# Performance work log

Measured on AMD Instinct MI355X. Metric: run time of the kernel, lower is better.

Reference implementation:

```python
import jax, jax.numpy as jnp
import numpy as np

B, S, D = 4, 2048, 16
N_HEAD_ARG = 16
# Faithful to source bug: effective num heads = hidden_size (D), head_size = D // n_head_arg.
# This only type-checks when head_size == 1 (D == n_head_arg), as in the repo config.
HEADS = D                     # self.n_head = hidden_size
HEAD_SIZE = D // N_HEAD_ARG   # = 1


def setup_inputs() -> dict:
    key = jax.random.key(0)
    k_x, k_wq, k_bq, k_wo, k_bo = jax.random.split(key, 5)
    x = jax.random.normal(k_x, (B, S, D), dtype=jnp.float32)
    # torch Linear init scale ~ 1/sqrt(in_features); store weights as [in, out]
    s = 1.0 / np.sqrt(D)
    w_qkv = jax.random.uniform(k_wq, (D, 3 * D), minval=-s, maxval=s, dtype=jnp.float32)
    b_qkv = jax.random.uniform(k_bq, (3 * D,), minval=-s, maxval=s, dtype=jnp.float32)
    w_out = jax.random.uniform(k_wo, (D, D), minval=-s, maxval=s, dtype=jnp.float32)
    b_out = jax.random.uniform(k_bo, (D,), minval=-s, maxval=s, dtype=jnp.float32)
    return {"x": x, "w_qkv": w_qkv, "b_qkv": b_qkv, "w_out": w_out, "b_out": b_out}


def reference(x, w_qkv, b_qkv, w_out, b_out):
    b, s, _ = x.shape
    qkv = x @ w_qkv + b_qkv                      # [b, s, 3D]
    q, k, v = jnp.split(qkv, 3, axis=-1)         # each [b, s, D]
    # [b, s, H, hs] -> [b, H, s, hs]
    q = q.reshape(b, s, HEADS, HEAD_SIZE).transpose(0, 2, 1, 3)
    k = k.reshape(b, s, HEADS, HEAD_SIZE).transpose(0, 2, 1, 3)
    v = v.reshape(b, s, HEADS, HEAD_SIZE).transpose(0, 2, 1, 3)
    scale = 1.0 / jnp.sqrt(jnp.asarray(HEAD_SIZE, dtype=x.dtype))
    scores = jnp.einsum('bhqd,bhkd->bhqk', q, k) * scale   # [b, H, s, s]
    causal = jnp.tril(jnp.ones((s, s), dtype=bool))
    scores = jnp.where(causal, scores, jnp.asarray(-jnp.inf, dtype=scores.dtype))
    attn = jax.nn.softmax(scores, axis=-1)
    # dropout is identity in eval mode (correctness baseline)
    out = jnp.einsum('bhqk,bhkd->bhqd', attn, v)            # [b, H, s, hs]
    out = out.transpose(0, 2, 1, 3).reshape(b, s, HEADS * HEAD_SIZE)
    return out @ w_out + b_out
```

## Files before the change

kernel.cpp:

```cpp
#include <hip/hip_runtime.h>
#include <math.h>

#define BB 4
#define SS 2048
#define DD 16
#define HH 16
#define NM 32

#define EXP2(x) __builtin_amdgcn_exp2f(x)
#define LOG2E 1.44269504088896340736f

__constant__ float INVFACT[NM] = {
    1.000000000e+00f, 1.000000000e+00f, 5.000000000e-01f, 1.666666667e-01f,
    4.166666667e-02f, 8.333333333e-03f, 1.388888889e-03f, 1.984126984e-04f,
    2.480158730e-05f, 2.755731922e-06f, 2.755731922e-07f, 2.505210839e-08f,
    2.087675699e-09f, 1.605904384e-10f, 1.147074560e-11f, 7.647163732e-13f,
    4.779477332e-14f, 2.811457254e-15f, 1.561920697e-16f, 8.220635247e-18f,
    4.110317623e-19f, 1.957294106e-20f, 8.896791392e-22f, 3.868170171e-23f,
    1.611737571e-24f, 6.446950284e-26f, 2.479596263e-27f, 9.183689864e-29f,
    3.279889237e-30f, 1.130996289e-31f, 3.769987629e-33f, 1.216125042e-34f};

#define UNPACK16(X4, XR)                                                   \
  const float4 x0_ = (X4)[0], x1_ = (X4)[1], x2_ = (X4)[2], x3_ = (X4)[3]; \
  const float XR[16] = {x0_.x, x0_.y, x0_.z, x0_.w, x1_.x, x1_.y, x1_.z,   \
                        x1_.w, x2_.x, x2_.y, x2_.z, x2_.w, x3_.x, x3_.y,   \
                        x3_.z, x3_.w};

__global__ __launch_bounds__(256) void moment_kernel(
    const float* __restrict__ x, const float* __restrict__ w_qkv,
    const float* __restrict__ b_qkv, float* __restrict__ MT) {
  __shared__ float kl[512];
  __shared__ float vl[512];
  const int blk = blockIdx.x;
  const int sub = blk & 3;
  const int bh = blk >> 2;
  const int b = bh >> 4, h = bh & 15;
  const int t = threadIdx.x;

  float wk[16], wv[16];
#pragma unroll
  for (int i = 0; i < 16; ++i) {
    wk[i] = w_qkv[i * 48 + 16 + h];
    wv[i] = w_qkv[i * 48 + 32 + h];
  }
  const float bk = b_qkv[16 + h], bv = b_qkv[32 + h];

#pragma unroll
  for (int rr = 0; rr < 2; ++rr) {
    const int jl = rr * 256 + t;
    const int j = sub * 512 + jl;
    const float4* X4 = (const float4*)(x + ((size_t)b * SS + j) * DD);
    UNPACK16(X4, xr);
    float k = bk, v = bv;
#pragma unroll
    for (int i = 0; i < 16; ++i) {
      k = fmaf(xr[i], wk[i], k);
      v = fmaf(xr[i], wv[i], v);
    }
    kl[jl] = k;
    vl[jl] = v;
  }
  __syncthreads();

  const int m = t & 31;
  const int jl = t >> 5;
  const int jb = sub * 8 + jl;
  float s = 0.f, tv = 0.f;
  const int base = jl * 64;
  for (int u = 0; u < 64; ++u) {
    const float k = kl[base + u];
    const float v = vl[base + u];
    const float k2 = k * k, k4 = k2 * k2, k8 = k4 * k4, k16 = k8 * k8;
    float p = (m & 1) ? k : 1.f;
    p *= (m & 2) ? k2 : 1.f;
    p *= (m & 4) ? k4 : 1.f;
    p *= (m & 8) ? k8 : 1.f;
    p *= (m & 16) ? k16 : 1.f;
    s += p;
    tv = fmaf(p, v, tv);
  }
  float* row = MT + ((size_t)bh * 32 + jb) * 64;
  row[m] = s;
  row[32 + m] = tv;
}

__global__ __launch_bounds__(64) void attn_kernel(
    const float* __restrict__ x, const float* __restrict__ w_qkv,
    const float* __restrict__ b_qkv, const float* __restrict__ MT,
    float* __restrict__ AO) {
  __shared__ float kd[64], vd[64], bc[64];
  const int blk = blockIdx.x;
  const int qb = blk & 31;
  const int bh = blk >> 5;
  const int b = bh >> 4, h = bh & 15;
  const int lane = threadIdx.x;

  float wq[16], wk[16], wv[16];
#pragma unroll
  for (int i = 0; i < 16; ++i) {
    wq[i] = w_qkv[i * 48 + h];
    wk[i] = w_qkv[i * 48 + 16 + h];
    wv[i] = w_qkv[i * 48 + 32 + h];
  }

  const int i0 = qb * 64 + lane;
  const float4* X4 = (const float4*)(x + ((size_t)b * SS + i0) * DD);
  UNPACK16(X4, xr);
  float q = b_qkv[h], k = b_qkv[16 + h], v = b_qkv[32 + h];
#pragma unroll
  for (int i = 0; i < 16; ++i) {
    q = fmaf(xr[i], wq[i], q);
    k = fmaf(xr[i], wk[i], k);
    v = fmaf(xr[i], wv[i], v);
  }
  kd[lane] = k;
  vd[lane] = v;
  const float qs = q * LOG2E;

  if (qb > 0) {
    const float* mtb = MT + (size_t)bh * 32 * 64 + lane;
    float acc = 0.f;
    for (int jb = 0; jb < qb; ++jb) acc += mtb[jb * 64];
    const float c = INVFACT[lane & 31];
    const int slot = (lane < 32) ? (2 * lane) : (2 * (lane - 32) + 1);
    bc[slot] = acc * c;
  }
  __syncthreads();

  float num = 0.f, den = 0.f;
  if (qb > 0) {
    const float2* bc2 = (const float2*)bc;
    float p = 1.f;
#pragma unroll
    for (int m = 0; m < NM; ++m) {
      const float2 st = bc2[m];
      den = fmaf(p, st.x, den);
      num = fmaf(p, st.y, num);
      p *= q;
    }
  }

  float ld = 0.f, ad = 0.f;
  const float4* kd4 = (const float4*)kd;
  const float4* vd4 = (const float4*)vd;
#pragma unroll
  for (int g = 0; g < 16; ++g) {
    const float4 k4 = kd4[g], v4 = vd4[g];
    const int jj = 4 * g;
    float e;
    e = EXP2(qs * k4.x); e = (jj + 0 <= lane) ? e : 0.f; ld += e; ad = fmaf(e, v4.x, ad);
    e = EXP2(qs * k4.y); e = (jj + 1 <= lane) ? e : 0.f; ld += e; ad = fmaf(e, v4.y, ad);
    e = EXP2(qs * k4.z); e = (jj + 2 <= lane) ? e : 0.f; ld += e; ad = fmaf(e, v4.z, ad);
    e = EXP2(qs * k4.w); e = (jj + 3 <= lane) ? e : 0.f; ld += e; ad = fmaf(e, v4.w, ad);
  }

  AO[(size_t)bh * SS + i0] = (ad + num) / (ld + den);
}

__global__ __launch_bounds__(256) void proj_kernel(
    const float* __restrict__ AO, const float* __restrict__ w,
    const float* __restrict__ bias, float* __restrict__ out) {
  __shared__ float wct[DD * 68];
  __shared__ float aol[256];
  __shared__ float bs[DD];
  const int t = threadIdx.x;
  const int b = blockIdx.x >> 7;
  const int s_base = (blockIdx.x * 16) & (SS - 1);

  wct[(t & 15) * 68 + (t >> 4)] = w[t];
  if (t < DD) bs[t] = bias[t];
  {
    const int h = t >> 4, row_l = t & 15;
    const int bh = b * HH + h;
    aol[row_l * 16 + h] = AO[(size_t)bh * SS + s_base + row_l];
  }
  __syncthreads();

  const int row_l = t >> 4, d = t & 15;
  const float4* ao4 = (const float4*)aol;
  const float4* wc4 = (const float4*)wct;

  float y = bs[d];
#pragma unroll
  for (int g = 0; g < 4; ++g) {
    const float4 xv = ao4[row_l * 4 + g];
    const float4 wv = wc4[d * 17 + g];
    y = fmaf(xv.x, wv.x, y);
    y = fmaf(xv.y, wv.y, y);
    y = fmaf(xv.z, wv.z, y);
    y = fmaf(xv.w, wv.w, y);
  }
  out[(size_t)blockIdx.x * 256 + t] = y;
}

extern "C" void kernel_launch(void* const* d_in, const int* in_sizes, int n_in,
                              void* d_out, int out_size, void* d_ws,
                              size_t ws_size, hipStream_t stream) {
  const float* x = (const float*)d_in[0];
  const float* w_qkv = (const float*)d_in[1];
  const float* b_qkv = (const float*)d_in[2];
  const float* w_out = (const float*)d_in[3];
  const float* b_out = (const float*)d_in[4];
  float* out = (float*)d_out;

  float* ws = (float*)d_ws;
  float* MT = ws;
  float* AO = ws + 64 * 32 * 64;

  moment_kernel<<<256, 256, 0, stream>>>(x, w_qkv, b_qkv, MT);
  attn_kernel<<<2048, 64, 0, stream>>>(x, w_qkv, b_qkv, MT, AO);
  proj_kernel<<<512, 256, 0, stream>>>(AO, w_out, b_out, out);
}
```

Baseline: 80.37 us.

## Fuse moment and attention kernels into one block per batch-head with LDS prefix scan

Merges the moment-computation kernel and the attention kernel into a single kernel where each 1024-thread block handles one (batch, head) pair. Q/K/V projections are computed once into shared memory, per-chunk Taylor moments are built there, and a Hillis-Steele prefix scan over chunks replaces the per-query-block global re-summation. This removes one launch, the MT round trip through global memory and the redundant recomputation of K/V per query block. The cost is only 64 blocks on a GPU with many more compute units, so most of the device sits idle.

```diff
diff --git a/kernel.cpp b/kernel.cpp
--- a/kernel.cpp
+++ b/kernel.cpp
@@ -26,135 +26,117 @@
                         x1_.w, x2_.x, x2_.y, x2_.z, x2_.w, x3_.x, x3_.y,   \
                         x3_.z, x3_.w};
 
-__global__ __launch_bounds__(256) void moment_kernel(
+__global__ __launch_bounds__(1024) void fused_attn_kernel(
     const float* __restrict__ x, const float* __restrict__ w_qkv,
-    const float* __restrict__ b_qkv, float* __restrict__ MT) {
-  __shared__ float kl[512];
-  __shared__ float vl[512];
-  const int blk = blockIdx.x;
-  const int sub = blk & 3;
-  const int bh = blk >> 2;
+    const float* __restrict__ b_qkv, float* __restrict__ AO) {
+  __shared__ float kl[SS];
+  __shared__ float vl[SS];
+  __shared__ float ql[SS];
+  __shared__ float2 SP[32 * 32];
+
+  const int bh = blockIdx.x;
   const int b = bh >> 4, h = bh & 15;
   const int t = threadIdx.x;
 
-  float wk[16], wv[16];
-#pragma unroll
-  for (int i = 0; i < 16; ++i) {
-    wk[i] = w_qkv[i * 48 + 16 + h];
-    wv[i] = w_qkv[i * 48 + 32 + h];
-  }
-  const float bk = b_qkv[16 + h], bv = b_qkv[32 + h];
-
-#pragma unroll
-  for (int rr = 0; rr < 2; ++rr) {
-    const int jl = rr * 256 + t;
-    const int j = sub * 512 + jl;
-    const float4* X4 = (const float4*)(x + ((size_t)b * SS + j) * DD);
-    UNPACK16(X4, xr);
-    float k = bk, v = bv;
+  {
+    float wq[16], wk[16], wv[16];
 #pragma unroll
     for (int i = 0; i < 16; ++i) {
-      k = fmaf(xr[i], wk[i], k);
-      v = fmaf(xr[i], wv[i], v);
+      wq[i] = w_qkv[i * 48 + h];
+      wk[i] = w_qkv[i * 48 + 16 + h];
+      wv[i] = w_qkv[i * 48 + 32 + h];
     }
-    kl[jl] = k;
-    vl[jl] = v;
+    const float bq = b_qkv[h], bk = b_qkv[16 + h], bv = b_qkv[32 + h];
+#pragma unroll
+    for (int rr = 0; rr < 2; ++rr) {
+      const int j = rr * 1024 + t;
+      const float4* X4 = (const float4*)(x + ((size_t)b * SS + j) * DD);
+      UNPACK16(X4, xr);
+      float qq = bq, kk = bk, vv = bv;
+#pragma unroll
+      for (int i = 0; i < 16; ++i) {
+        qq = fmaf(xr[i], wq[i], qq);
+        kk = fmaf(xr[i], wk[i], kk);
+        vv = fmaf(xr[i], wv[i], vv);
+      }
+      ql[j] = qq;
+      kl[j] = kk;
+      vl[j] = vv;
+    }
   }
   __syncthreads();
 
-  const int m = t & 31;
-  const int jl = t >> 5;
-  const int jb = sub * 8 + jl;
-  float s = 0.f, tv = 0.f;
-  const int base = jl * 64;
-  for (int u = 0; u < 64; ++u) {
-    const float k = kl[base + u];
-    const float v = vl[base + u];
-    const float k2 = k * k, k4 = k2 * k2, k8 = k4 * k4, k16 = k8 * k8;
-    float p = (m & 1) ? k : 1.f;
-    p *= (m & 2) ? k2 : 1.f;
-    p *= (m & 4) ? k4 : 1.f;
-    p *= (m & 8) ? k8 : 1.f;
-    p *= (m & 16) ? k16 : 1.f;
-    s += p;
-    tv = fmaf(p, v, tv);
-  }
-  float* row = MT + ((size_t)bh * 32 + jb) * 64;
-  row[m] = s;
-  row[32 + m] = tv;
-}
-
-__global__ __launch_bounds__(64) void attn_kernel(
-    const float* __restrict__ x, const float* __restrict__ w_qkv,
-    const float* __restrict__ b_qkv, const float* __restrict__ MT,
-    float* __restrict__ AO) {
-  __shared__ float kd[64], vd[64], bc[64];
-  const int blk = blockIdx.x;
-  const int qb = blk & 31;
-  const int bh = blk >> 5;
-  const int b = bh >> 4, h = bh & 15;
-  const int lane = threadIdx.x;
-
-  float wq[16], wk[16], wv[16];
-#pragma unroll
-  for (int i = 0; i < 16; ++i) {
-    wq[i] = w_qkv[i * 48 + h];
-    wk[i] = w_qkv[i * 48 + 16 + h];
-    wv[i] = w_qkv[i * 48 + 32 + h];
-  }
-
-  const int i0 = qb * 64 + lane;
-  const float4* X4 = (const float4*)(x + ((size_t)b * SS + i0) * DD);
-  UNPACK16(X4, xr);
-  float q = b_qkv[h], k = b_qkv[16 + h], v = b_qkv[32 + h];
-#pragma unroll
-  for (int i = 0; i < 16; ++i) {
-    q = fmaf(xr[i], wq[i], q);
-    k = fmaf(xr[i], wk[i], k);
-    v = fmaf(xr[i], wv[i], v);
-  }
-  kd[lane] = k;
-  vd[lane] = v;
-  const float qs = q * LOG2E;
-
-  if (qb > 0) {
-    const float* mtb = MT + (size_t)bh * 32 * 64 + lane;
-    float acc = 0.f;
-    for (int jb = 0; jb < qb; ++jb) acc += mtb[jb * 64];
-    const float c = INVFACT[lane & 31];
-    const int slot = (lane < 32) ? (2 * lane) : (2 * (lane - 32) + 1);
-    bc[slot] = acc * c;
+  {
+    const int m = t & 31;
+    const int jb = t >> 5;
+    const float c = INVFACT[m];
+    float s = 0.f, tv = 0.f;
+    const int base = jb * 64;
+    for (int u = 0; u < 64; ++u) {
+      const float k = kl[base + u];
+      const float v = vl[base + u];
+      const float k2 = k * k, k4 = k2 * k2, k8 = k4 * k4, k16 = k8 * k8;
+      float p = (m & 1) ? k : 1.f;
+      p *= (m & 2) ? k2 : 1.f;
+      p *= (m & 4) ? k4 : 1.f;
+      p *= (m & 8) ? k8 : 1.f;
+      p *= (m & 16) ? k16 : 1.f;
+      s += p;
+      tv = fmaf(p, v, tv);
+    }
+    SP[t] = make_float2(s * c, tv * c);
   }
   __syncthreads();
 
-  float num = 0.f, den = 0.f;
-  if (qb > 0) {
-    const float2* bc2 = (const float2*)bc;
-    float p = 1.f;
+  {
+    const int jb = t >> 5;
 #pragma unroll
-    for (int m = 0; m < NM; ++m) {
-      const float2 st = bc2[m];
-      den = fmaf(p, st.x, den);
-      num = fmaf(p, st.y, num);
-      p *= q;
+    for (int off = 1; off < 32; off <<= 1) {
+      const float2 self = SP[t];
+      float2 othr = make_float2(0.f, 0.f);
+      if (jb >= off) othr = SP[t - off * 32];
+      __syncthreads();
+      SP[t] = make_float2(self.x + othr.x, self.y + othr.y);
+      __syncthreads();
     }
   }
 
-  float ld = 0.f, ad = 0.f;
-  const float4* kd4 = (const float4*)kd;
-  const float4* vd4 = (const float4*)vd;
+  for (int rr = 0; rr < 2; ++rr) {
+    const int i = rr * 1024 + t;
+    const int lane = i & 63;
+    const int qb = i >> 6;
+    const float q = ql[i];
+    const float qs = q * LOG2E;
+
+    float num = 0.f, den = 0.f;
+    if (qb > 0) {
+      const float2* bc2 = SP + (size_t)(qb - 1) * 32;
+      float p = 1.f;
 #pragma unroll
-  for (int g = 0; g < 16; ++g) {
-    const float4 k4 = kd4[g], v4 = vd4[g];
-    const int jj = 4 * g;
-    float e;
-    e = EXP2(qs * k4.x); e = (jj + 0 <= lane) ? e : 0.f; ld += e; ad = fmaf(e, v4.x, ad);
-    e = EXP2(qs * k4.y); e = (jj + 1 <= lane) ? e : 0.f; ld += e; ad = fmaf(e, v4.y, ad);
-    e = EXP2(qs * k4.z); e = (jj + 2 <= lane) ? e : 0.f; ld += e; ad = fmaf(e, v4.z, ad);
-    e = EXP2(qs * k4.w); e = (jj + 3 <= lane) ? e : 0.f; ld += e; ad = fmaf(e, v4.w, ad);
+      for (int m = 0; m < NM; ++m) {
+        const float2 st = bc2[m];
+        den = fmaf(p, st.x, den);
+        num = fmaf(p, st.y, num);
+        p *= q;
+      }
+    }
+
+    float ld = 0.f, ad = 0.f;
+    const float4* kd4 = (const float4*)(kl + qb * 64);
+    const float4* vd4 = (const float4*)(vl + qb * 64);
+#pragma unroll
+    for (int g = 0; g < 16; ++g) {
+      const float4 k4 = kd4[g], v4 = vd4[g];
+      const int jj = 4 * g;
+      float e;
+      e = EXP2(qs * k4.x); e = (jj + 0 <= lane) ? e : 0.f; ld += e; ad = fmaf(e, v4.x, ad);
+      e = EXP2(qs * k4.y); e = (jj + 1 <= lane) ? e : 0.f; ld += e; ad = fmaf(e, v4.y, ad);
+      e = EXP2(qs * k4.z); e = (jj + 2 <= lane) ? e : 0.f; ld += e; ad = fmaf(e, v4.z, ad);
+      e = EXP2(qs * k4.w); e = (jj + 3 <= lane) ? e : 0.f; ld += e; ad = fmaf(e, v4.w, ad);
+    }
+
+    AO[(size_t)bh * SS + i] = (ad + num) / (ld + den);
   }
-
-  AO[(size_t)bh * SS + i0] = (ad + num) / (ld + den);
 }
 
 __global__ __launch_bounds__(256) void proj_kernel(
@@ -203,11 +185,8 @@
   const float* b_out = (const float*)d_in[4];
   float* out = (float*)d_out;
 
-  float* ws = (float*)d_ws;
-  float* MT = ws;
-  float* AO = ws + 64 * 32 * 64;
+  float* AO = (float*)d_ws;
 
-  moment_kernel<<<256, 256, 0, stream>>>(x, w_qkv, b_qkv, MT);
-  attn_kernel<<<2048, 64, 0, stream>>>(x, w_qkv, b_qkv, MT, AO);
+  fused_attn_kernel<<<64, 1024, 0, stream>>>(x, w_qkv, b_qkv, AO);
   proj_kernel<<<512, 256, 0, stream>>>(AO, w_out, b_out, out);
 }
```

Result: faster. 77.61 us (-3.4%).
